# Kernel optimization log

Hardware: AMD Instinct MI355X
Metric: run time of the kernel (lower is better)

Reference implementation:

```python
import jax, jax.numpy as jnp
import numpy as np
import math

N_HEADS = 8
D_E = 64


def setup_inputs() -> dict:
    key = jax.random.key(0)
    k1, k2, k3 = jax.random.split(key, 3)
    B, C, L = 4, 512, 2048
    x = jax.random.normal(k1, (B, C, L), dtype=jnp.float32)
    # 1x1-conv (channel-mixing) projection shared by Q and K (the original
    # uses query_conv for both Q and K).
    W_q = jax.random.normal(k2, (N_HEADS * D_E, C), dtype=jnp.float32) * 0.02
    b_q = jax.random.normal(k3, (N_HEADS * D_E,), dtype=jnp.float32) * 0.02
    return {"x": x, "W_q": W_q, "b_q": b_q}


def reference(x, W_q, b_q):
    B, C, L = x.shape
    H, d_e = N_HEADS, D_E
    # 1x1 conv over channels: (B, H*d_e, L)
    qk = jnp.einsum('oc,bcl->bol', W_q, x) + b_q[None, :, None]
    # (B, H, L, d_e); K == Q per the original (both use query_conv)
    Q = qk.reshape(B, H, d_e, L).transpose(0, 1, 3, 2)
    K = Q
    scores = jnp.einsum('bhqd,bhkd->bhqk', Q, K) / math.sqrt(d_e)
    # causal mask: positions k > q masked to -inf (triu(diagonal=1) masked)
    causal = jnp.arange(L)[None, :] <= jnp.arange(L)[:, None]  # (L, L)
    scores = jnp.where(causal[None, None], scores, -jnp.inf)
    A = jax.nn.softmax(scores, axis=-1)  # (B, H, L, L)
    # values are the raw input sequence, (B, L, C)
    V = x.transpose(0, 2, 1)
    H_att = jnp.einsum('bhqk,bkc->bhqc', A, V)  # (B, H, L, C)
    out = H_att + V[:, None]                      # residual add per head
    # -> (B, H*C, L)
    return out.transpose(0, 1, 3, 2).reshape(B, H * C, L)
```

## Files before the change

kernel.cpp:

```cpp
#include <hip/hip_runtime.h>
#include <hip/hip_bf16.h>

#define B_ 4
#define C_ 512
#define L_ 2048
#define H_ 8
#define E_ 64
#define QSCALE 0.4246609f
#define NUNITS 1024

typedef __attribute__((ext_vector_type(8))) short bf16x8;
typedef __attribute__((ext_vector_type(4))) float f32x4;
typedef __attribute__((ext_vector_type(4))) unsigned short u16x4;

static __device__ __forceinline__ unsigned short f2bf(float f) {
    union { float f; unsigned u; } v; v.f = f;
    unsigned r = v.u + 0x7FFFu + ((v.u >> 16) & 1u);
    return (unsigned short)(r >> 16);
}

#define LBAR() do { asm volatile("s_waitcnt lgkmcnt(0)" ::: "memory"); \
                    __builtin_amdgcn_s_barrier(); } while (0)

__global__ __launch_bounds__(256) void prep_kernel(const float* __restrict__ x,
                                                   unsigned short* __restrict__ xb,
                                                   unsigned short* __restrict__ xt) {
    const int lt = blockIdx.x, ct = blockIdx.y, b = blockIdx.z;
    const int l0 = lt * 64, c0 = ct * 64;
    const int t = threadIdx.x;
    __shared__ unsigned short T[64 * 72];

    const int cl = t >> 2, lo = (t & 3) * 16;
    const float* src = x + ((size_t)(b * C_ + c0 + cl)) * L_ + l0 + lo;
    unsigned short u[16];
    #pragma unroll
    for (int j = 0; j < 16; j += 4) {
        float4 v = *reinterpret_cast<const float4*>(src + j);
        u[j] = f2bf(v.x); u[j + 1] = f2bf(v.y); u[j + 2] = f2bf(v.z); u[j + 3] = f2bf(v.w);
    }
    unsigned short* xbp = xb + ((size_t)(b * C_ + c0 + cl)) * L_ + l0 + lo;
    reinterpret_cast<uint4*>(xbp)[0] = reinterpret_cast<uint4*>(u)[0];
    reinterpret_cast<uint4*>(xbp)[1] = reinterpret_cast<uint4*>(u)[1];
    reinterpret_cast<uint4*>(&T[cl * 72 + lo])[0] = reinterpret_cast<uint4*>(u)[0];
    reinterpret_cast<uint4*>(&T[cl * 72 + lo + 8])[0] = reinterpret_cast<uint4*>(u)[1];
    __syncthreads();
    const int ll = t >> 2, co = (t & 3) * 16;
    unsigned short v16[16];
    #pragma unroll
    for (int j = 0; j < 16; ++j) v16[j] = T[(co + j) * 72 + ll];
    unsigned short* xtp = xt + ((size_t)b * L_ + l0 + ll) * C_ + c0 + co;
    reinterpret_cast<uint4*>(xtp)[0] = reinterpret_cast<uint4*>(v16)[0];
    reinterpret_cast<uint4*>(xtp)[1] = reinterpret_cast<uint4*>(v16)[1];
}

__global__ __launch_bounds__(256) void wcast_kernel(const float* __restrict__ W,
                                                    unsigned short* __restrict__ Wb) {
    const int i = blockIdx.x * 256 + threadIdx.x;
    float4 v = reinterpret_cast<const float4*>(W)[i];
    union { unsigned short u[4]; unsigned long long ll; } o;
    o.u[0] = f2bf(v.x); o.u[1] = f2bf(v.y); o.u[2] = f2bf(v.z); o.u[3] = f2bf(v.w);
    reinterpret_cast<unsigned long long*>(Wb)[i] = o.ll;
}

__global__ __launch_bounds__(256) void proj_kernel(const unsigned short* __restrict__ Wb,
                                                   const float* __restrict__ bq,
                                                   const unsigned short* __restrict__ xt,
                                                   unsigned short* __restrict__ qb) {
    const int lt = blockIdx.x, h = blockIdx.y, b = blockIdx.z;
    const int tid = threadIdx.x, w = tid >> 6, lane = tid & 63;
    const int lr = lane & 15, lg = lane >> 4;
    const int l = lt * 64 + w * 16 + lr;
    const int o0 = h * 64;

    f32x4 acc[4] = {};
    const unsigned short* xrow = xt + ((size_t)b * L_ + l) * C_;
    for (int ks = 0; ks < 16; ++ks) {
        bf16x8 bf = *reinterpret_cast<const bf16x8*>(xrow + ks * 32 + lg * 8);
        #pragma unroll
        for (int mt = 0; mt < 4; ++mt) {
            bf16x8 af = *reinterpret_cast<const bf16x8*>(Wb + (size_t)(o0 + mt * 16 + lr) * C_ + ks * 32 + lg * 8);
            acc[mt] = __builtin_amdgcn_mfma_f32_16x16x32_bf16(af, bf, acc[mt], 0, 0, 0);
        }
    }
    const int bh = b * H_ + h;
    unsigned short* qrow = qb + ((size_t)bh * L_ + l) * 64;
    #pragma unroll
    for (int mt = 0; mt < 4; ++mt) {
        const int e0 = mt * 16 + lg * 4;
        const float4 bb = *reinterpret_cast<const float4*>(bq + o0 + e0);
        union { unsigned short u[4]; unsigned long long ll; } o;
        o.u[0] = f2bf((acc[mt][0] + bb.x) * QSCALE);
        o.u[1] = f2bf((acc[mt][1] + bb.y) * QSCALE);
        o.u[2] = f2bf((acc[mt][2] + bb.z) * QSCALE);
        o.u[3] = f2bf((acc[mt][3] + bb.w) * QSCALE);
        *reinterpret_cast<unsigned long long*>(qrow + e0) = o.ll;
    }
}

#define LDV(KS)                                                                       \
    {                                                                                 \
        _Pragma("unroll")                                                             \
        for (int ct = 0; ct < 4; ++ct)                                                \
            pvv[ct] = *reinterpret_cast<const bf16x8*>(                               \
                Vbase + (size_t)(c0w + ct * 16 + lr) * L_ + k0 + (KS) * 32 + lg * 8); \
    }

#define PV_USE(KS)                                                                    \
    {                                                                                 \
        bf16x8 pa[4];                                                                 \
        _Pragma("unroll")                                                             \
        for (int mt = 0; mt < 4; ++mt) {                                              \
            const int row = mt * 16 + lr;                                             \
            const int g2 = ((KS) * 4 + lg) ^ lr;                                      \
            pa[mt] = *reinterpret_cast<const bf16x8*>(&Pb[row * 128 + (g2 << 3)]);    \
        }                                                                             \
        __builtin_amdgcn_s_setprio(1);                                                \
        _Pragma("unroll")                                                             \
        for (int mt = 0; mt < 4; ++mt)                                                \
            _Pragma("unroll")                                                         \
            for (int ct = 0; ct < 4; ++ct)                                            \
                acc[mt][ct] = __builtin_amdgcn_mfma_f32_16x16x32_bf16(                \
                    pa[mt], pvv[ct], acc[mt][ct], 0, 0, 0);                           \
        __builtin_amdgcn_s_setprio(0);                                                \
    }

__global__ __launch_bounds__(512, 4) void pv_kernel(const unsigned short* __restrict__ qb,
                                                    const unsigned short* __restrict__ xb,
                                                    float* __restrict__ out,
                                                    int* __restrict__ counter) {
    const int tid = threadIdx.x, w = tid >> 6, lane = tid & 63;
    const int lr = lane & 15, lg = lane >> 4;
    const int c0w = w * 64;

    __shared__ unsigned short Qt[64 * 64];
    __shared__ unsigned short P2[2][64 * 128];
    __shared__ float rsT[64][8];
    __shared__ int s_u;

    for (;;) {
        __syncthreads();
        if (tid == 0) s_u = atomicAdd(counter, 1);
        __syncthreads();
        const int u = s_u;
        if (u >= NUNITS) return;

        const int qt = 31 - (u >> 5);
        const int rr = u & 31;
        const int b = rr >> 3, h = rr & 7;
        const int q0 = qt * 64, qlim = q0 + 63;
        const int nkt = (q0 >> 7) + 1;
        const int bh = b * H_ + h;
        const unsigned short* Qbase = qb + (size_t)bh * L_ * 64;
        const unsigned short* Vbase = xb + (size_t)b * C_ * L_;

        {
            const int r = tid >> 3, g = tid & 7;
            bf16x8 v = *reinterpret_cast<const bf16x8*>(Qbase + (size_t)(q0 + r) * 64 + g * 8);
            *reinterpret_cast<bf16x8*>(&Qt[r * 64 + ((g ^ (r & 7)) << 3)]) = v;
        }

        bf16x8 pvv[4];
        f32x4 acc[4][4] = {};
        float rs[4] = {0.f, 0.f, 0.f, 0.f};

        LBAR();

        #pragma unroll 1
        for (int kt = 0; kt < nkt; ++kt) {
            const int k0 = kt * 128;
            const int ksmax = min(4, ((qlim - k0) >> 5) + 1);
            unsigned short* Pb = (unsigned short*)P2[kt & 1];
            const bool active = (k0 + (w & ~1) * 16) <= qlim;

            LDV(0)

            if (active) {
                const size_t krow = (size_t)(k0 + w * 16 + lr) * 64;
                bf16x8 kb0 = *reinterpret_cast<const bf16x8*>(Qbase + krow + lg * 8);
                bf16x8 kb1 = *reinterpret_cast<const bf16x8*>(Qbase + krow + 32 + lg * 8);
                f32x4 z[4];
                #pragma unroll
                for (int nt = 0; nt < 4; ++nt) {
                    bf16x8 aq0 = *reinterpret_cast<const bf16x8*>(&Qt[(nt * 16 + lr) * 64 + ((lg ^ (lr & 7)) << 3)]);
                    bf16x8 aq1 = *reinterpret_cast<const bf16x8*>(&Qt[(nt * 16 + lr) * 64 + (((4 + lg) ^ (lr & 7)) << 3)]);
                    f32x4 zz = {};
                    zz = __builtin_amdgcn_mfma_f32_16x16x32_bf16(kb0, aq0, zz, 0, 0, 0);
                    zz = __builtin_amdgcn_mfma_f32_16x16x32_bf16(kb1, aq1, zz, 0, 0, 0);
                    z[nt] = zz;
                }
                const int kbase = k0 + w * 16 + lg * 4;
                #pragma unroll
                for (int nt = 0; nt < 4; ++nt) {
                    const int q = q0 + nt * 16 + lr;
                    const float p0 = (kbase + 0 <= q) ? exp2f(z[nt][0]) : 0.f;
                    const float p1 = (kbase + 1 <= q) ? exp2f(z[nt][1]) : 0.f;
                    const float p2 = (kbase + 2 <= q) ? exp2f(z[nt][2]) : 0.f;
                    const float p3 = (kbase + 3 <= q) ? exp2f(z[nt][3]) : 0.f;
                    rs[nt] += (p0 + p1) + (p2 + p3);
                    unsigned r01, r23;
                    asm("v_cvt_pk_bf16_f32 %0, %1, %2" : "=v"(r01) : "v"(p0), "v"(p1));
                    asm("v_cvt_pk_bf16_f32 %0, %1, %2" : "=v"(r23) : "v"(p2), "v"(p3));
                    const int row = nt * 16 + lr;
                    const int col = w * 16 + lg * 4;
                    const int gg = (col >> 3) ^ lr;
                    const unsigned long long pk = ((unsigned long long)r23 << 32) | r01;
                    *reinterpret_cast<unsigned long long*>(&Pb[row * 128 + (gg << 3) + (col & 7)]) = pk;
                }
            }
            LBAR();

            PV_USE(0)
            LDV(1)
            PV_USE(1)
            if (ksmax == 4) {
                LDV(2)
                PV_USE(2)
                LDV(3)
                PV_USE(3)
            }
        }

        #pragma unroll
        for (int nt = 0; nt < 4; ++nt) {
            float t0 = __shfl_xor(rs[nt], 16); rs[nt] += t0;
            float t1 = __shfl_xor(rs[nt], 32); rs[nt] += t1;
        }
        if (lg == 0) {
            #pragma unroll
            for (int nt = 0; nt < 4; ++nt) rsT[nt * 16 + lr][w] = rs[nt];
        }
        LBAR();
        float li[16];
        #pragma unroll
        for (int mt = 0; mt < 4; ++mt)
            #pragma unroll
            for (int r = 0; r < 4; ++r) {
                const int row = mt * 16 + lg * 4 + r;
                const f32x4 s0 = *reinterpret_cast<const f32x4*>(&rsT[row][0]);
                const f32x4 s1 = *reinterpret_cast<const f32x4*>(&rsT[row][4]);
                li[mt * 4 + r] = 1.f / (((s0[0] + s0[1]) + (s0[2] + s0[3])) + ((s1[0] + s1[1]) + (s1[2] + s1[3])));
            }

        const unsigned short* xres = xb + (size_t)b * C_ * L_;
        float* ob = out + (size_t)bh * C_ * L_;
        #pragma unroll
        for (int ct = 0; ct < 4; ++ct) {
            const int c = c0w + ct * 16 + lr;
            #pragma unroll
            for (int mt = 0; mt < 4; ++mt) {
                const int lbase = q0 + mt * 16 + lg * 4;
                const u16x4 rv = __builtin_nontemporal_load(
                    reinterpret_cast<const u16x4*>(xres + (size_t)c * L_ + lbase));
                f32x4 o;
                o[0] = acc[mt][ct][0] * li[mt * 4 + 0] + __uint_as_float((unsigned)rv[0] << 16);
                o[1] = acc[mt][ct][1] * li[mt * 4 + 1] + __uint_as_float((unsigned)rv[1] << 16);
                o[2] = acc[mt][ct][2] * li[mt * 4 + 2] + __uint_as_float((unsigned)rv[2] << 16);
                o[3] = acc[mt][ct][3] * li[mt * 4 + 3] + __uint_as_float((unsigned)rv[3] << 16);
                __builtin_nontemporal_store(o, reinterpret_cast<f32x4*>(ob + (size_t)c * L_ + lbase));
            }
        }
    }
}

extern "C" void kernel_launch(void* const* d_in, const int* in_sizes, int n_in,
                              void* d_out, int out_size, void* d_ws, size_t ws_size,
                              hipStream_t stream) {
    const float* x  = (const float*)d_in[0];
    const float* Wq = (const float*)d_in[1];
    const float* bq = (const float*)d_in[2];
    float* out = (float*)d_out;

    unsigned short* xb   = (unsigned short*)d_ws;
    unsigned short* xt   = xb + (size_t)B_ * C_ * L_;
    unsigned short* qbuf = xt + (size_t)B_ * L_ * C_;
    unsigned short* Wb   = qbuf + (size_t)B_ * H_ * L_ * E_;
    int* counter = (int*)(Wb + (size_t)H_ * E_ * C_);

    (void)hipMemsetAsync(counter, 0, 4, stream);
    prep_kernel<<<dim3(32, 8, 4), 256, 0, stream>>>(x, xb, xt);
    wcast_kernel<<<dim3(256), 256, 0, stream>>>(Wq, Wb);
    proj_kernel<<<dim3(32, 8, 4), 256, 0, stream>>>(Wb, bq, xt, qbuf);
    pv_kernel<<<dim3(768), 512, 0, stream>>>(qbuf, xb, out, counter);
}
```

Baseline: 290.5 us.

## Double attention query tile to 128 rows using 1024-thread blocks

The fused score/PV kernel now handles 128 query rows per work unit with 16 waves instead of 64 rows with 8 waves. Each wave covers 32 channels over all 128 rows, so every V tile loaded from global memory is reused across twice as many queries. The causal-diagonal partial-tile logic is dropped, so diagonal tiles are computed in full with masking. The larger shared-memory footprint and 1024-thread blocks lower the number of resident blocks per CU, and the grid shrinks to 256 persistent blocks.

```diff
diff --git a/kernel.cpp b/kernel.cpp
--- a/kernel.cpp
+++ b/kernel.cpp
@@ -7,7 +7,7 @@
 #define H_ 8
 #define E_ 64
 #define QSCALE 0.4246609f
-#define NUNITS 1024
+#define NUNITS 512
 
 typedef __attribute__((ext_vector_type(8))) short bf16x8;
 typedef __attribute__((ext_vector_type(4))) float f32x4;
@@ -97,44 +97,49 @@
     }
 }
 
-#define LDV(KS)                                                                       \
-    {                                                                                 \
-        _Pragma("unroll")                                                             \
-        for (int ct = 0; ct < 4; ++ct)                                                \
-            pvv[ct] = *reinterpret_cast<const bf16x8*>(                               \
-                Vbase + (size_t)(c0w + ct * 16 + lr) * L_ + k0 + (KS) * 32 + lg * 8); \
-    }
-
-#define PV_USE(KS)                                                                    \
-    {                                                                                 \
-        bf16x8 pa[4];                                                                 \
-        _Pragma("unroll")                                                             \
-        for (int mt = 0; mt < 4; ++mt) {                                              \
-            const int row = mt * 16 + lr;                                             \
-            const int g2 = ((KS) * 4 + lg) ^ lr;                                      \
-            pa[mt] = *reinterpret_cast<const bf16x8*>(&Pb[row * 128 + (g2 << 3)]);    \
-        }                                                                             \
-        __builtin_amdgcn_s_setprio(1);                                                \
-        _Pragma("unroll")                                                             \
-        for (int mt = 0; mt < 4; ++mt)                                                \
-            _Pragma("unroll")                                                         \
-            for (int ct = 0; ct < 4; ++ct)                                            \
-                acc[mt][ct] = __builtin_amdgcn_mfma_f32_16x16x32_bf16(                \
-                    pa[mt], pvv[ct], acc[mt][ct], 0, 0, 0);                           \
-        __builtin_amdgcn_s_setprio(0);                                                \
-    }
-
-__global__ __launch_bounds__(512, 4) void pv_kernel(const unsigned short* __restrict__ qb,
-                                                    const unsigned short* __restrict__ xb,
-                                                    float* __restrict__ out,
-                                                    int* __restrict__ counter) {
+#define LDV(KS)                                                                        \
+    {                                                                                  \
+        _Pragma("unroll")                                                              \
+        for (int ct = 0; ct < 2; ++ct)                                                 \
+            pvv[ct] = *reinterpret_cast<const bf16x8*>(                                \
+                Vbase + (size_t)(c0w + ct * 16 + lr) * L_ + k0 + (KS) * 32 + lg * 8);  \
+    }
+
+#define PV_USE(KS)                                                                     \
+    {                                                                                  \
+        _Pragma("unroll")                                                              \
+        for (int half = 0; half < 2; ++half) {                                         \
+            bf16x8 pa[4];                                                              \
+            _Pragma("unroll")                                                          \
+            for (int mt = 0; mt < 4; ++mt) {                                           \
+                const int row = half * 64 + mt * 16 + lr;                              \
+                const int g2 = ((KS) * 4 + lg) ^ lr;                                   \
+                pa[mt] = *reinterpret_cast<const bf16x8*>(&Pb[row * 128 + (g2 << 3)]); \
+            }                                                                          \
+            __builtin_amdgcn_s_setprio(1);                                             \
+            _Pragma("unroll")                                                          \
+            for (int mt = 0; mt < 4; ++mt)                                             \
+                _Pragma("unroll")                                                      \
+                for (int ct = 0; ct < 2; ++ct)                                         \
+                    acc[half * 4 + mt][ct] = __builtin_amdgcn_mfma_f32_16x16x32_bf16(  \
+                        pa[mt], pvv[ct], acc[half * 4 + mt][ct], 0, 0, 0);             \
+            __builtin_amdgcn_s_setprio(0);                                             \
+        }                                                                              \
+    }
+
+__global__ __launch_bounds__(1024, 4) void pv_kernel(const unsigned short* __restrict__ qb,
+                                                     const unsigned short* __restrict__ xb,
+                                                     float* __restrict__ out,
+                                                     int* __restrict__ counter) {
     const int tid = threadIdx.x, w = tid >> 6, lane = tid & 63;
     const int lr = lane & 15, lg = lane >> 4;
-    const int c0w = w * 64;
-
-    __shared__ unsigned short Qt[64 * 64];
-    __shared__ unsigned short P2[2][64 * 128];
-    __shared__ float rsT[64][8];
+    const int sq = w >> 3;
+    const int wk = w & 7;
+    const int c0w = w * 32;
+
+    __shared__ unsigned short Qt[128 * 64];
+    __shared__ unsigned short P2[2][128 * 128];
+    __shared__ float rsT[128][8];
     __shared__ int s_u;
 
     for (;;) {
@@ -144,11 +149,11 @@
         const int u = s_u;
         if (u >= NUNITS) return;
 
-        const int qt = 31 - (u >> 5);
+        const int qt = 15 - (u >> 5);
         const int rr = u & 31;
         const int b = rr >> 3, h = rr & 7;
-        const int q0 = qt * 64, qlim = q0 + 63;
-        const int nkt = (q0 >> 7) + 1;
+        const int q0 = qt * 128;
+        const int nkt = qt + 1;
         const int bh = b * H_ + h;
         const unsigned short* Qbase = qb + (size_t)bh * L_ * 64;
         const unsigned short* Vbase = xb + (size_t)b * C_ * L_;
@@ -159,8 +164,8 @@
             *reinterpret_cast<bf16x8*>(&Qt[r * 64 + ((g ^ (r & 7)) << 3)]) = v;
         }
 
-        bf16x8 pvv[4];
-        f32x4 acc[4][4] = {};
+        bf16x8 pvv[2];
+        f32x4 acc[8][2] = {};
         float rs[4] = {0.f, 0.f, 0.f, 0.f};
 
         LBAR();
@@ -168,56 +173,45 @@
         #pragma unroll 1
         for (int kt = 0; kt < nkt; ++kt) {
             const int k0 = kt * 128;
-            const int ksmax = min(4, ((qlim - k0) >> 5) + 1);
             unsigned short* Pb = (unsigned short*)P2[kt & 1];
-            const bool active = (k0 + (w & ~1) * 16) <= qlim;
-
+
+            const size_t krow = (size_t)(k0 + wk * 16 + lr) * 64;
+            bf16x8 kb0 = *reinterpret_cast<const bf16x8*>(Qbase + krow + lg * 8);
+            bf16x8 kb1 = *reinterpret_cast<const bf16x8*>(Qbase + krow + 32 + lg * 8);
             LDV(0)
 
-            if (active) {
-                const size_t krow = (size_t)(k0 + w * 16 + lr) * 64;
-                bf16x8 kb0 = *reinterpret_cast<const bf16x8*>(Qbase + krow + lg * 8);
-                bf16x8 kb1 = *reinterpret_cast<const bf16x8*>(Qbase + krow + 32 + lg * 8);
-                f32x4 z[4];
-                #pragma unroll
-                for (int nt = 0; nt < 4; ++nt) {
-                    bf16x8 aq0 = *reinterpret_cast<const bf16x8*>(&Qt[(nt * 16 + lr) * 64 + ((lg ^ (lr & 7)) << 3)]);
-                    bf16x8 aq1 = *reinterpret_cast<const bf16x8*>(&Qt[(nt * 16 + lr) * 64 + (((4 + lg) ^ (lr & 7)) << 3)]);
-                    f32x4 zz = {};
-                    zz = __builtin_amdgcn_mfma_f32_16x16x32_bf16(kb0, aq0, zz, 0, 0, 0);
-                    zz = __builtin_amdgcn_mfma_f32_16x16x32_bf16(kb1, aq1, zz, 0, 0, 0);
-                    z[nt] = zz;
-                }
-                const int kbase = k0 + w * 16 + lg * 4;
-                #pragma unroll
-                for (int nt = 0; nt < 4; ++nt) {
-                    const int q = q0 + nt * 16 + lr;
-                    const float p0 = (kbase + 0 <= q) ? exp2f(z[nt][0]) : 0.f;
-                    const float p1 = (kbase + 1 <= q) ? exp2f(z[nt][1]) : 0.f;
-                    const float p2 = (kbase + 2 <= q) ? exp2f(z[nt][2]) : 0.f;
-                    const float p3 = (kbase + 3 <= q) ? exp2f(z[nt][3]) : 0.f;
-                    rs[nt] += (p0 + p1) + (p2 + p3);
-                    unsigned r01, r23;
-                    asm("v_cvt_pk_bf16_f32 %0, %1, %2" : "=v"(r01) : "v"(p0), "v"(p1));
-                    asm("v_cvt_pk_bf16_f32 %0, %1, %2" : "=v"(r23) : "v"(p2), "v"(p3));
-                    const int row = nt * 16 + lr;
-                    const int col = w * 16 + lg * 4;
-                    const int gg = (col >> 3) ^ lr;
-                    const unsigned long long pk = ((unsigned long long)r23 << 32) | r01;
-                    *reinterpret_cast<unsigned long long*>(&Pb[row * 128 + (gg << 3) + (col & 7)]) = pk;
-                }
+            const int kbase = k0 + wk * 16 + lg * 4;
+            #pragma unroll
+            for (int nt = 0; nt < 4; ++nt) {
+                const int qrow = sq * 64 + nt * 16 + lr;
+                bf16x8 aq0 = *reinterpret_cast<const bf16x8*>(&Qt[qrow * 64 + ((lg ^ (lr & 7)) << 3)]);
+                bf16x8 aq1 = *reinterpret_cast<const bf16x8*>(&Qt[qrow * 64 + (((4 + lg) ^ (lr & 7)) << 3)]);
+                f32x4 z = {};
+                z = __builtin_amdgcn_mfma_f32_16x16x32_bf16(kb0, aq0, z, 0, 0, 0);
+                z = __builtin_amdgcn_mfma_f32_16x16x32_bf16(kb1, aq1, z, 0, 0, 0);
+                const int q = q0 + qrow;
+                const float p0 = (kbase + 0 <= q) ? exp2f(z[0]) : 0.f;
+                const float p1 = (kbase + 1 <= q) ? exp2f(z[1]) : 0.f;
+                const float p2 = (kbase + 2 <= q) ? exp2f(z[2]) : 0.f;
+                const float p3 = (kbase + 3 <= q) ? exp2f(z[3]) : 0.f;
+                rs[nt] += (p0 + p1) + (p2 + p3);
+                unsigned r01, r23;
+                asm("v_cvt_pk_bf16_f32 %0, %1, %2" : "=v"(r01) : "v"(p0), "v"(p1));
+                asm("v_cvt_pk_bf16_f32 %0, %1, %2" : "=v"(r23) : "v"(p2), "v"(p3));
+                const int col = wk * 16 + lg * 4;
+                const int gg = (col >> 3) ^ lr;
+                const unsigned long long pk = ((unsigned long long)r23 << 32) | r01;
+                *reinterpret_cast<unsigned long long*>(&Pb[qrow * 128 + (gg << 3) + (col & 7)]) = pk;
             }
             LBAR();
 
             PV_USE(0)
             LDV(1)
             PV_USE(1)
-            if (ksmax == 4) {
-                LDV(2)
-                PV_USE(2)
-                LDV(3)
-                PV_USE(3)
-            }
+            LDV(2)
+            PV_USE(2)
+            LDV(3)
+            PV_USE(3)
         }
 
         #pragma unroll
@@ -227,35 +221,33 @@
         }
         if (lg == 0) {
             #pragma unroll
-            for (int nt = 0; nt < 4; ++nt) rsT[nt * 16 + lr][w] = rs[nt];
+            for (int nt = 0; nt < 4; ++nt) rsT[sq * 64 + nt * 16 + lr][wk] = rs[nt];
         }
         LBAR();
-        float li[16];
-        #pragma unroll
-        for (int mt = 0; mt < 4; ++mt)
-            #pragma unroll
-            for (int r = 0; r < 4; ++r) {
-                const int row = mt * 16 + lg * 4 + r;
-                const f32x4 s0 = *reinterpret_cast<const f32x4*>(&rsT[row][0]);
-                const f32x4 s1 = *reinterpret_cast<const f32x4*>(&rsT[row][4]);
-                li[mt * 4 + r] = 1.f / (((s0[0] + s0[1]) + (s0[2] + s0[3])) + ((s1[0] + s1[1]) + (s1[2] + s1[3])));
-            }
 
         const unsigned short* xres = xb + (size_t)b * C_ * L_;
         float* ob = out + (size_t)bh * C_ * L_;
         #pragma unroll
-        for (int ct = 0; ct < 4; ++ct) {
-            const int c = c0w + ct * 16 + lr;
-            #pragma unroll
-            for (int mt = 0; mt < 4; ++mt) {
-                const int lbase = q0 + mt * 16 + lg * 4;
+        for (int mt = 0; mt < 8; ++mt) {
+            const int rowb = mt * 16 + lg * 4;
+            f32x4 li;
+            #pragma unroll
+            for (int r = 0; r < 4; ++r) {
+                const f32x4 s0 = *reinterpret_cast<const f32x4*>(&rsT[rowb + r][0]);
+                const f32x4 s1 = *reinterpret_cast<const f32x4*>(&rsT[rowb + r][4]);
+                li[r] = 1.f / (((s0[0] + s0[1]) + (s0[2] + s0[3])) + ((s1[0] + s1[1]) + (s1[2] + s1[3])));
+            }
+            const int lbase = q0 + rowb;
+            #pragma unroll
+            for (int ct = 0; ct < 2; ++ct) {
+                const int c = c0w + ct * 16 + lr;
                 const u16x4 rv = __builtin_nontemporal_load(
                     reinterpret_cast<const u16x4*>(xres + (size_t)c * L_ + lbase));
                 f32x4 o;
-                o[0] = acc[mt][ct][0] * li[mt * 4 + 0] + __uint_as_float((unsigned)rv[0] << 16);
-                o[1] = acc[mt][ct][1] * li[mt * 4 + 1] + __uint_as_float((unsigned)rv[1] << 16);
-                o[2] = acc[mt][ct][2] * li[mt * 4 + 2] + __uint_as_float((unsigned)rv[2] << 16);
-                o[3] = acc[mt][ct][3] * li[mt * 4 + 3] + __uint_as_float((unsigned)rv[3] << 16);
+                o[0] = acc[mt][ct][0] * li[0] + __uint_as_float((unsigned)rv[0] << 16);
+                o[1] = acc[mt][ct][1] * li[1] + __uint_as_float((unsigned)rv[1] << 16);
+                o[2] = acc[mt][ct][2] * li[2] + __uint_as_float((unsigned)rv[2] << 16);
+                o[3] = acc[mt][ct][3] * li[3] + __uint_as_float((unsigned)rv[3] << 16);
                 __builtin_nontemporal_store(o, reinterpret_cast<f32x4*>(ob + (size_t)c * L_ + lbase));
             }
         }
@@ -280,5 +272,5 @@
     prep_kernel<<<dim3(32, 8, 4), 256, 0, stream>>>(x, xb, xt);
     wcast_kernel<<<dim3(256), 256, 0, stream>>>(Wq, Wb);
     proj_kernel<<<dim3(32, 8, 4), 256, 0, stream>>>(Wb, bq, xt, qbuf);
-    pv_kernel<<<dim3(768), 512, 0, stream>>>(qbuf, xb, out, counter);
-}
+    pv_kernel<<<dim3(256), 1024, 0, stream>>>(qbuf, xb, out, counter);
+}
```

New measurement: 287.5 us. Within noise of the previous version (-1.0%).

## Split attention work units across channel halves with 4-wave blocks

Applied to the files above, without the earlier changes.

The fused attention kernel now assigns each work unit to one (batch, head, query tile, channel half), doubling the unit count and using 256-thread blocks with four waves. Each wave computes 32 key columns of the score tile instead of 16, and the double-buffered P tile is replaced by a single buffer with an extra barrier after the PV step. This aims to improve load balance and occupancy under the persistent atomic scheduler. In exchange the QK^T scores and exponentials are recomputed twice per query tile, once per channel half.

```diff
diff --git a/kernel.cpp b/kernel.cpp
--- a/kernel.cpp
+++ b/kernel.cpp
@@ -7,7 +7,7 @@
 #define H_ 8
 #define E_ 64
 #define QSCALE 0.4246609f
-#define NUNITS 1024
+#define NUNITS 2048
 
 typedef __attribute__((ext_vector_type(8))) short bf16x8;
 typedef __attribute__((ext_vector_type(4))) float f32x4;
@@ -97,44 +97,40 @@
     }
 }
 
-#define LDV(KS)                                                                       \
-    {                                                                                 \
-        _Pragma("unroll")                                                             \
-        for (int ct = 0; ct < 4; ++ct)                                                \
-            pvv[ct] = *reinterpret_cast<const bf16x8*>(                               \
-                Vbase + (size_t)(c0w + ct * 16 + lr) * L_ + k0 + (KS) * 32 + lg * 8); \
-    }
-
-#define PV_USE(KS)                                                                    \
-    {                                                                                 \
-        bf16x8 pa[4];                                                                 \
-        _Pragma("unroll")                                                             \
-        for (int mt = 0; mt < 4; ++mt) {                                              \
-            const int row = mt * 16 + lr;                                             \
-            const int g2 = ((KS) * 4 + lg) ^ lr;                                      \
-            pa[mt] = *reinterpret_cast<const bf16x8*>(&Pb[row * 128 + (g2 << 3)]);    \
-        }                                                                             \
-        __builtin_amdgcn_s_setprio(1);                                                \
-        _Pragma("unroll")                                                             \
-        for (int mt = 0; mt < 4; ++mt)                                                \
-            _Pragma("unroll")                                                         \
-            for (int ct = 0; ct < 4; ++ct)                                            \
-                acc[mt][ct] = __builtin_amdgcn_mfma_f32_16x16x32_bf16(                \
-                    pa[mt], pvv[ct], acc[mt][ct], 0, 0, 0);                           \
-        __builtin_amdgcn_s_setprio(0);                                                \
-    }
-
-__global__ __launch_bounds__(512, 4) void pv_kernel(const unsigned short* __restrict__ qb,
+#define PV_STEP(S)                                                                        \
+    {                                                                                     \
+        bf16x8 vf[4];                                                                     \
+        _Pragma("unroll")                                                                 \
+        for (int ct = 0; ct < 4; ++ct)                                                    \
+            vf[ct] = *reinterpret_cast<const bf16x8*>(                                    \
+                Vbase + (size_t)(c0w + ct * 16 + lr) * L_ + k0 + (S) * 32 + lg * 8);      \
+        bf16x8 pa[4];                                                                     \
+        _Pragma("unroll")                                                                 \
+        for (int qs = 0; qs < 4; ++qs) {                                                  \
+            const int row = qs * 16 + lr;                                                 \
+            const int g2 = ((S) * 4 + lg) ^ (lr & 7);                                     \
+            pa[qs] = *reinterpret_cast<const bf16x8*>(&P[row * 128 + (g2 << 3)]);         \
+        }                                                                                 \
+        __builtin_amdgcn_s_setprio(1);                                                    \
+        _Pragma("unroll")                                                                 \
+        for (int qs = 0; qs < 4; ++qs)                                                    \
+            _Pragma("unroll")                                                             \
+            for (int ct = 0; ct < 4; ++ct)                                                \
+                acc[qs][ct] = __builtin_amdgcn_mfma_f32_16x16x32_bf16(                    \
+                    pa[qs], vf[ct], acc[qs][ct], 0, 0, 0);                                \
+        __builtin_amdgcn_s_setprio(0);                                                    \
+    }
+
+__global__ __launch_bounds__(256, 4) void pv_kernel(const unsigned short* __restrict__ qb,
                                                     const unsigned short* __restrict__ xb,
                                                     float* __restrict__ out,
                                                     int* __restrict__ counter) {
     const int tid = threadIdx.x, w = tid >> 6, lane = tid & 63;
     const int lr = lane & 15, lg = lane >> 4;
-    const int c0w = w * 64;
 
     __shared__ unsigned short Qt[64 * 64];
-    __shared__ unsigned short P2[2][64 * 128];
-    __shared__ float rsT[64][8];
+    __shared__ unsigned short P[64 * 128];
+    __shared__ float rsT[64][4];
     __shared__ int s_u;
 
     for (;;) {
@@ -144,22 +140,26 @@
         const int u = s_u;
         if (u >= NUNITS) return;
 
-        const int qt = 31 - (u >> 5);
-        const int rr = u & 31;
-        const int b = rr >> 3, h = rr & 7;
+        const int qt = 31 - (u >> 6);
+        const int rr = u & 63;
+        const int bh = rr >> 1, ch = rr & 1;
+        const int b = bh >> 3;
         const int q0 = qt * 64, qlim = q0 + 63;
         const int nkt = (q0 >> 7) + 1;
-        const int bh = b * H_ + h;
+        const int c0w = ch * 256 + w * 64;
         const unsigned short* Qbase = qb + (size_t)bh * L_ * 64;
         const unsigned short* Vbase = xb + (size_t)b * C_ * L_;
 
         {
-            const int r = tid >> 3, g = tid & 7;
-            bf16x8 v = *reinterpret_cast<const bf16x8*>(Qbase + (size_t)(q0 + r) * 64 + g * 8);
-            *reinterpret_cast<bf16x8*>(&Qt[r * 64 + ((g ^ (r & 7)) << 3)]) = v;
-        }
-
-        bf16x8 pvv[4];
+            const int r = tid >> 2, seg = tid & 3;
+            const unsigned short* src = Qbase + (size_t)(q0 + r) * 64 + seg * 16;
+            bf16x8 v0 = *reinterpret_cast<const bf16x8*>(src);
+            bf16x8 v1 = *reinterpret_cast<const bf16x8*>(src + 8);
+            const int g0 = seg * 2, g1 = seg * 2 + 1;
+            *reinterpret_cast<bf16x8*>(&Qt[r * 64 + ((g0 ^ (r & 7)) << 3)]) = v0;
+            *reinterpret_cast<bf16x8*>(&Qt[r * 64 + ((g1 ^ (r & 7)) << 3)]) = v1;
+        }
+
         f32x4 acc[4][4] = {};
         float rs[4] = {0.f, 0.f, 0.f, 0.f};
 
@@ -169,93 +169,87 @@
         for (int kt = 0; kt < nkt; ++kt) {
             const int k0 = kt * 128;
             const int ksmax = min(4, ((qlim - k0) >> 5) + 1);
-            unsigned short* Pb = (unsigned short*)P2[kt & 1];
-            const bool active = (k0 + (w & ~1) * 16) <= qlim;
-
-            LDV(0)
+            const bool active = (w < ksmax);
+            const int kw0 = k0 + w * 32;
 
             if (active) {
-                const size_t krow = (size_t)(k0 + w * 16 + lr) * 64;
-                bf16x8 kb0 = *reinterpret_cast<const bf16x8*>(Qbase + krow + lg * 8);
-                bf16x8 kb1 = *reinterpret_cast<const bf16x8*>(Qbase + krow + 32 + lg * 8);
-                f32x4 z[4];
+                bf16x8 kb[2][2];
                 #pragma unroll
-                for (int nt = 0; nt < 4; ++nt) {
-                    bf16x8 aq0 = *reinterpret_cast<const bf16x8*>(&Qt[(nt * 16 + lr) * 64 + ((lg ^ (lr & 7)) << 3)]);
-                    bf16x8 aq1 = *reinterpret_cast<const bf16x8*>(&Qt[(nt * 16 + lr) * 64 + (((4 + lg) ^ (lr & 7)) << 3)]);
-                    f32x4 zz = {};
-                    zz = __builtin_amdgcn_mfma_f32_16x16x32_bf16(kb0, aq0, zz, 0, 0, 0);
-                    zz = __builtin_amdgcn_mfma_f32_16x16x32_bf16(kb1, aq1, zz, 0, 0, 0);
-                    z[nt] = zz;
+                for (int ksub = 0; ksub < 2; ++ksub) {
+                    const size_t krow = (size_t)(kw0 + ksub * 16 + lr) * 64;
+                    kb[ksub][0] = *reinterpret_cast<const bf16x8*>(Qbase + krow + lg * 8);
+                    kb[ksub][1] = *reinterpret_cast<const bf16x8*>(Qbase + krow + 32 + lg * 8);
                 }
-                const int kbase = k0 + w * 16 + lg * 4;
                 #pragma unroll
-                for (int nt = 0; nt < 4; ++nt) {
-                    const int q = q0 + nt * 16 + lr;
-                    const float p0 = (kbase + 0 <= q) ? exp2f(z[nt][0]) : 0.f;
-                    const float p1 = (kbase + 1 <= q) ? exp2f(z[nt][1]) : 0.f;
-                    const float p2 = (kbase + 2 <= q) ? exp2f(z[nt][2]) : 0.f;
-                    const float p3 = (kbase + 3 <= q) ? exp2f(z[nt][3]) : 0.f;
-                    rs[nt] += (p0 + p1) + (p2 + p3);
-                    unsigned r01, r23;
-                    asm("v_cvt_pk_bf16_f32 %0, %1, %2" : "=v"(r01) : "v"(p0), "v"(p1));
-                    asm("v_cvt_pk_bf16_f32 %0, %1, %2" : "=v"(r23) : "v"(p2), "v"(p3));
-                    const int row = nt * 16 + lr;
-                    const int col = w * 16 + lg * 4;
-                    const int gg = (col >> 3) ^ lr;
-                    const unsigned long long pk = ((unsigned long long)r23 << 32) | r01;
-                    *reinterpret_cast<unsigned long long*>(&Pb[row * 128 + (gg << 3) + (col & 7)]) = pk;
+                for (int qs = 0; qs < 4; ++qs) {
+                    const int qrow = qs * 16 + lr;
+                    bf16x8 qf0 = *reinterpret_cast<const bf16x8*>(&Qt[qrow * 64 + ((lg ^ (qrow & 7)) << 3)]);
+                    bf16x8 qf1 = *reinterpret_cast<const bf16x8*>(&Qt[qrow * 64 + (((4 + lg) ^ (qrow & 7)) << 3)]);
+                    const int q = q0 + qrow;
+                    #pragma unroll
+                    for (int ksub = 0; ksub < 2; ++ksub) {
+                        f32x4 z = {};
+                        z = __builtin_amdgcn_mfma_f32_16x16x32_bf16(kb[ksub][0], qf0, z, 0, 0, 0);
+                        z = __builtin_amdgcn_mfma_f32_16x16x32_bf16(kb[ksub][1], qf1, z, 0, 0, 0);
+                        const int kbase = kw0 + ksub * 16 + lg * 4;
+                        const float p0 = (kbase + 0 <= q) ? exp2f(z[0]) : 0.f;
+                        const float p1 = (kbase + 1 <= q) ? exp2f(z[1]) : 0.f;
+                        const float p2 = (kbase + 2 <= q) ? exp2f(z[2]) : 0.f;
+                        const float p3 = (kbase + 3 <= q) ? exp2f(z[3]) : 0.f;
+                        rs[qs] += (p0 + p1) + (p2 + p3);
+                        unsigned r01, r23;
+                        asm("v_cvt_pk_bf16_f32 %0, %1, %2" : "=v"(r01) : "v"(p0), "v"(p1));
+                        asm("v_cvt_pk_bf16_f32 %0, %1, %2" : "=v"(r23) : "v"(p2), "v"(p3));
+                        const int kl = w * 32 + ksub * 16 + lg * 4;
+                        const int g = (kl >> 3) ^ (qrow & 7);
+                        const unsigned long long pk = ((unsigned long long)r23 << 32) | r01;
+                        *reinterpret_cast<unsigned long long*>(&P[qrow * 128 + (g << 3) + (kl & 7)]) = pk;
+                    }
                 }
             }
             LBAR();
 
-            PV_USE(0)
-            LDV(1)
-            PV_USE(1)
+            PV_STEP(0)
+            PV_STEP(1)
             if (ksmax == 4) {
-                LDV(2)
-                PV_USE(2)
-                LDV(3)
-                PV_USE(3)
-            }
+                PV_STEP(2)
+                PV_STEP(3)
+            }
+            LBAR();
         }
 
         #pragma unroll
-        for (int nt = 0; nt < 4; ++nt) {
-            float t0 = __shfl_xor(rs[nt], 16); rs[nt] += t0;
-            float t1 = __shfl_xor(rs[nt], 32); rs[nt] += t1;
+        for (int qs = 0; qs < 4; ++qs) {
+            float t0 = __shfl_xor(rs[qs], 16); rs[qs] += t0;
+            float t1 = __shfl_xor(rs[qs], 32); rs[qs] += t1;
         }
         if (lg == 0) {
             #pragma unroll
-            for (int nt = 0; nt < 4; ++nt) rsT[nt * 16 + lr][w] = rs[nt];
+            for (int qs = 0; qs < 4; ++qs) rsT[qs * 16 + lr][w] = rs[qs];
         }
         LBAR();
-        float li[16];
-        #pragma unroll
-        for (int mt = 0; mt < 4; ++mt)
-            #pragma unroll
-            for (int r = 0; r < 4; ++r) {
-                const int row = mt * 16 + lg * 4 + r;
-                const f32x4 s0 = *reinterpret_cast<const f32x4*>(&rsT[row][0]);
-                const f32x4 s1 = *reinterpret_cast<const f32x4*>(&rsT[row][4]);
-                li[mt * 4 + r] = 1.f / (((s0[0] + s0[1]) + (s0[2] + s0[3])) + ((s1[0] + s1[1]) + (s1[2] + s1[3])));
-            }
 
         const unsigned short* xres = xb + (size_t)b * C_ * L_;
         float* ob = out + (size_t)bh * C_ * L_;
         #pragma unroll
-        for (int ct = 0; ct < 4; ++ct) {
-            const int c = c0w + ct * 16 + lr;
+        for (int qs = 0; qs < 4; ++qs) {
+            f32x4 li;
             #pragma unroll
-            for (int mt = 0; mt < 4; ++mt) {
-                const int lbase = q0 + mt * 16 + lg * 4;
+            for (int r = 0; r < 4; ++r) {
+                const f32x4 s4 = *reinterpret_cast<const f32x4*>(&rsT[qs * 16 + lg * 4 + r][0]);
+                li[r] = 1.f / ((s4[0] + s4[1]) + (s4[2] + s4[3]));
+            }
+            const int lbase = q0 + qs * 16 + lg * 4;
+            #pragma unroll
+            for (int ct = 0; ct < 4; ++ct) {
+                const int c = c0w + ct * 16 + lr;
                 const u16x4 rv = __builtin_nontemporal_load(
                     reinterpret_cast<const u16x4*>(xres + (size_t)c * L_ + lbase));
                 f32x4 o;
-                o[0] = acc[mt][ct][0] * li[mt * 4 + 0] + __uint_as_float((unsigned)rv[0] << 16);
-                o[1] = acc[mt][ct][1] * li[mt * 4 + 1] + __uint_as_float((unsigned)rv[1] << 16);
-                o[2] = acc[mt][ct][2] * li[mt * 4 + 2] + __uint_as_float((unsigned)rv[2] << 16);
-                o[3] = acc[mt][ct][3] * li[mt * 4 + 3] + __uint_as_float((unsigned)rv[3] << 16);
+                o[0] = acc[qs][ct][0] * li[0] + __uint_as_float((unsigned)rv[0] << 16);
+                o[1] = acc[qs][ct][1] * li[1] + __uint_as_float((unsigned)rv[1] << 16);
+                o[2] = acc[qs][ct][2] * li[2] + __uint_as_float((unsigned)rv[2] << 16);
+                o[3] = acc[qs][ct][3] * li[3] + __uint_as_float((unsigned)rv[3] << 16);
                 __builtin_nontemporal_store(o, reinterpret_cast<f32x4*>(ob + (size_t)c * L_ + lbase));
             }
         }
@@ -280,5 +274,5 @@
     prep_kernel<<<dim3(32, 8, 4), 256, 0, stream>>>(x, xb, xt);
     wcast_kernel<<<dim3(256), 256, 0, stream>>>(Wq, Wb);
     proj_kernel<<<dim3(32, 8, 4), 256, 0, stream>>>(Wb, bq, xt, qbuf);
-    pv_kernel<<<dim3(768), 512, 0, stream>>>(qbuf, xb, out, counter);
-}
+    pv_kernel<<<dim3(1024), 256, 0, stream>>>(qbuf, xb, out, counter);
+}
```

Measured after the change: 379.8 us. 1.31x slower.

## Warp-specialize pv_kernel into score-producer and PV-consumer waves with double buffering

Applied to the files above, without the earlier changes.

Splits each 768-thread block into 4 producer waves, which compute QK^T scores, exp and row sums into a double-buffered P tile one k-tile ahead, and 8 consumer waves, which run the PV MFMAs and the epilogue. Consumer V loads are also double-buffered in registers so the next slice is prefetched during the current MFMAs. The aim is to overlap the softmax/score stage with the PV matmul rather than serializing them each iteration. In exchange, the grid drops to 256 persistent blocks with launch bounds 768,3, which changes occupancy and register limits, and block-wide barriers still couple the two roles.

```diff
diff --git a/kernel.cpp b/kernel.cpp
--- a/kernel.cpp
+++ b/kernel.cpp
@@ -97,44 +97,91 @@
     }
 }
 
-#define LDV(KS)                                                                       \
-    {                                                                                 \
-        _Pragma("unroll")                                                             \
-        for (int ct = 0; ct < 4; ++ct)                                                \
-            pvv[ct] = *reinterpret_cast<const bf16x8*>(                               \
-                Vbase + (size_t)(c0w + ct * 16 + lr) * L_ + k0 + (KS) * 32 + lg * 8); \
-    }
-
-#define PV_USE(KS)                                                                    \
-    {                                                                                 \
-        bf16x8 pa[4];                                                                 \
-        _Pragma("unroll")                                                             \
-        for (int mt = 0; mt < 4; ++mt) {                                              \
-            const int row = mt * 16 + lr;                                             \
-            const int g2 = ((KS) * 4 + lg) ^ lr;                                      \
-            pa[mt] = *reinterpret_cast<const bf16x8*>(&Pb[row * 128 + (g2 << 3)]);    \
-        }                                                                             \
-        __builtin_amdgcn_s_setprio(1);                                                \
-        _Pragma("unroll")                                                             \
-        for (int mt = 0; mt < 4; ++mt)                                                \
-            _Pragma("unroll")                                                         \
-            for (int ct = 0; ct < 4; ++ct)                                            \
-                acc[mt][ct] = __builtin_amdgcn_mfma_f32_16x16x32_bf16(                \
-                    pa[mt], pvv[ct], acc[mt][ct], 0, 0, 0);                           \
-        __builtin_amdgcn_s_setprio(0);                                                \
-    }
-
-__global__ __launch_bounds__(512, 4) void pv_kernel(const unsigned short* __restrict__ qb,
+#define PRODUCE(BUF, PK0)                                                                        \
+    {                                                                                            \
+        const int kw0 = (PK0) + sw * 32;                                                         \
+        if (kw0 <= qlim) {                                                                       \
+            bf16x8 kb00, kb01, kb10, kb11;                                                       \
+            {                                                                                    \
+                const size_t kr0 = (size_t)(kw0 + lr) * 64;                                      \
+                const size_t kr1 = (size_t)(kw0 + 16 + lr) * 64;                                 \
+                kb00 = *reinterpret_cast<const bf16x8*>(Qbase + kr0 + lg * 8);                   \
+                kb01 = *reinterpret_cast<const bf16x8*>(Qbase + kr0 + 32 + lg * 8);              \
+                kb10 = *reinterpret_cast<const bf16x8*>(Qbase + kr1 + lg * 8);                   \
+                kb11 = *reinterpret_cast<const bf16x8*>(Qbase + kr1 + 32 + lg * 8);              \
+            }                                                                                    \
+            unsigned short* Pw = (unsigned short*)P2[BUF];                                       \
+            _Pragma("unroll")                                                                    \
+            for (int nt = 0; nt < 4; ++nt) {                                                     \
+                const int qrow = nt * 16 + lr;                                                   \
+                bf16x8 aq0 = *reinterpret_cast<const bf16x8*>(&Qt[qrow * 64 + ((lg ^ (lr & 7)) << 3)]);       \
+                bf16x8 aq1 = *reinterpret_cast<const bf16x8*>(&Qt[qrow * 64 + (((4 + lg) ^ (lr & 7)) << 3)]); \
+                const int q = q0 + qrow;                                                         \
+                _Pragma("unroll")                                                                \
+                for (int ksub = 0; ksub < 2; ++ksub) {                                           \
+                    f32x4 z = {};                                                                \
+                    z = __builtin_amdgcn_mfma_f32_16x16x32_bf16(ksub ? kb10 : kb00, aq0, z, 0, 0, 0); \
+                    z = __builtin_amdgcn_mfma_f32_16x16x32_bf16(ksub ? kb11 : kb01, aq1, z, 0, 0, 0); \
+                    const int kbase = kw0 + ksub * 16 + lg * 4;                                  \
+                    const float p0 = (kbase + 0 <= q) ? exp2f(z[0]) : 0.f;                       \
+                    const float p1 = (kbase + 1 <= q) ? exp2f(z[1]) : 0.f;                       \
+                    const float p2 = (kbase + 2 <= q) ? exp2f(z[2]) : 0.f;                       \
+                    const float p3 = (kbase + 3 <= q) ? exp2f(z[3]) : 0.f;                       \
+                    rs[nt] += (p0 + p1) + (p2 + p3);                                             \
+                    unsigned r01, r23;                                                           \
+                    asm("v_cvt_pk_bf16_f32 %0, %1, %2" : "=v"(r01) : "v"(p0), "v"(p1));          \
+                    asm("v_cvt_pk_bf16_f32 %0, %1, %2" : "=v"(r23) : "v"(p2), "v"(p3));          \
+                    const int kl = sw * 32 + ksub * 16 + lg * 4;                                 \
+                    const int gg = (kl >> 3) ^ lr;                                               \
+                    const unsigned long long pk = ((unsigned long long)r23 << 32) | r01;         \
+                    *reinterpret_cast<unsigned long long*>(&Pw[qrow * 128 + (gg << 3) + (kl & 7)]) = pk; \
+                }                                                                                \
+            }                                                                                    \
+        }                                                                                        \
+    }
+
+#define LDVB(BANK, KOFF)                                                                \
+    {                                                                                   \
+        _Pragma("unroll")                                                               \
+        for (int ct = 0; ct < 4; ++ct)                                                  \
+            pvv[BANK][ct] = *reinterpret_cast<const bf16x8*>(                           \
+                Vbase + (size_t)(c0w + ct * 16 + lr) * L_ + (KOFF) + lg * 8);           \
+    }
+
+#define PV_STEP(CUR, NXT, S)                                                            \
+    {                                                                                   \
+        const int nl = ((S) + 1 < ksmax) ? k0 + ((S) + 1) * 32 : k0 + 128;              \
+        LDVB(NXT, nl)                                                                   \
+        bf16x8 pa[4];                                                                   \
+        _Pragma("unroll")                                                               \
+        for (int mt = 0; mt < 4; ++mt) {                                                \
+            const int row = mt * 16 + lr;                                               \
+            const int g2 = ((S) * 4 + lg) ^ lr;                                         \
+            pa[mt] = *reinterpret_cast<const bf16x8*>(&Pb[row * 128 + (g2 << 3)]);      \
+        }                                                                               \
+        __builtin_amdgcn_s_setprio(1);                                                  \
+        _Pragma("unroll")                                                               \
+        for (int mt = 0; mt < 4; ++mt)                                                  \
+            _Pragma("unroll")                                                           \
+            for (int ct = 0; ct < 4; ++ct)                                              \
+                acc[mt][ct] = __builtin_amdgcn_mfma_f32_16x16x32_bf16(                  \
+                    pa[mt], pvv[CUR][ct], acc[mt][ct], 0, 0, 0);                        \
+        __builtin_amdgcn_s_setprio(0);                                                  \
+    }
+
+__global__ __launch_bounds__(768, 3) void pv_kernel(const unsigned short* __restrict__ qb,
                                                     const unsigned short* __restrict__ xb,
                                                     float* __restrict__ out,
                                                     int* __restrict__ counter) {
     const int tid = threadIdx.x, w = tid >> 6, lane = tid & 63;
     const int lr = lane & 15, lg = lane >> 4;
-    const int c0w = w * 64;
+    const bool isS = (w < 4);
+    const int sw = w;
+    const int c0w = (w - 4) * 64;
 
     __shared__ unsigned short Qt[64 * 64];
     __shared__ unsigned short P2[2][64 * 128];
-    __shared__ float rsT[64][8];
+    __shared__ float rsT[64][4];
     __shared__ int s_u;
 
     for (;;) {
@@ -153,110 +200,80 @@
         const unsigned short* Qbase = qb + (size_t)bh * L_ * 64;
         const unsigned short* Vbase = xb + (size_t)b * C_ * L_;
 
-        {
+        if (tid < 512) {
             const int r = tid >> 3, g = tid & 7;
             bf16x8 v = *reinterpret_cast<const bf16x8*>(Qbase + (size_t)(q0 + r) * 64 + g * 8);
             *reinterpret_cast<bf16x8*>(&Qt[r * 64 + ((g ^ (r & 7)) << 3)]) = v;
         }
 
-        bf16x8 pvv[4];
         f32x4 acc[4][4] = {};
         float rs[4] = {0.f, 0.f, 0.f, 0.f};
-
+        bf16x8 pvv[2][4];
+
+        LBAR();
+
+        if (isS) {
+            PRODUCE(0, 0)
+        } else {
+            LDVB(0, 0)
+        }
         LBAR();
 
         #pragma unroll 1
         for (int kt = 0; kt < nkt; ++kt) {
             const int k0 = kt * 128;
-            const int ksmax = min(4, ((qlim - k0) >> 5) + 1);
-            unsigned short* Pb = (unsigned short*)P2[kt & 1];
-            const bool active = (k0 + (w & ~1) * 16) <= qlim;
-
-            LDV(0)
-
-            if (active) {
-                const size_t krow = (size_t)(k0 + w * 16 + lr) * 64;
-                bf16x8 kb0 = *reinterpret_cast<const bf16x8*>(Qbase + krow + lg * 8);
-                bf16x8 kb1 = *reinterpret_cast<const bf16x8*>(Qbase + krow + 32 + lg * 8);
-                f32x4 z[4];
-                #pragma unroll
-                for (int nt = 0; nt < 4; ++nt) {
-                    bf16x8 aq0 = *reinterpret_cast<const bf16x8*>(&Qt[(nt * 16 + lr) * 64 + ((lg ^ (lr & 7)) << 3)]);
-                    bf16x8 aq1 = *reinterpret_cast<const bf16x8*>(&Qt[(nt * 16 + lr) * 64 + (((4 + lg) ^ (lr & 7)) << 3)]);
-                    f32x4 zz = {};
-                    zz = __builtin_amdgcn_mfma_f32_16x16x32_bf16(kb0, aq0, zz, 0, 0, 0);
-                    zz = __builtin_amdgcn_mfma_f32_16x16x32_bf16(kb1, aq1, zz, 0, 0, 0);
-                    z[nt] = zz;
-                }
-                const int kbase = k0 + w * 16 + lg * 4;
-                #pragma unroll
-                for (int nt = 0; nt < 4; ++nt) {
-                    const int q = q0 + nt * 16 + lr;
-                    const float p0 = (kbase + 0 <= q) ? exp2f(z[nt][0]) : 0.f;
-                    const float p1 = (kbase + 1 <= q) ? exp2f(z[nt][1]) : 0.f;
-                    const float p2 = (kbase + 2 <= q) ? exp2f(z[nt][2]) : 0.f;
-                    const float p3 = (kbase + 3 <= q) ? exp2f(z[nt][3]) : 0.f;
-                    rs[nt] += (p0 + p1) + (p2 + p3);
-                    unsigned r01, r23;
-                    asm("v_cvt_pk_bf16_f32 %0, %1, %2" : "=v"(r01) : "v"(p0), "v"(p1));
-                    asm("v_cvt_pk_bf16_f32 %0, %1, %2" : "=v"(r23) : "v"(p2), "v"(p3));
-                    const int row = nt * 16 + lr;
-                    const int col = w * 16 + lg * 4;
-                    const int gg = (col >> 3) ^ lr;
-                    const unsigned long long pk = ((unsigned long long)r23 << 32) | r01;
-                    *reinterpret_cast<unsigned long long*>(&Pb[row * 128 + (gg << 3) + (col & 7)]) = pk;
+            if (isS) {
+                if (kt + 1 < nkt) PRODUCE((kt + 1) & 1, k0 + 128)
+            } else {
+                const unsigned short* Pb = (const unsigned short*)P2[kt & 1];
+                const int ksmax = min(4, ((qlim - k0) >> 5) + 1);
+                PV_STEP(0, 1, 0)
+                PV_STEP(1, 0, 1)
+                if (ksmax == 4) {
+                    PV_STEP(0, 1, 2)
+                    PV_STEP(1, 0, 3)
                 }
             }
             LBAR();
-
-            PV_USE(0)
-            LDV(1)
-            PV_USE(1)
-            if (ksmax == 4) {
-                LDV(2)
-                PV_USE(2)
-                LDV(3)
-                PV_USE(3)
+        }
+
+        if (isS) {
+            #pragma unroll
+            for (int nt = 0; nt < 4; ++nt) {
+                float t0 = __shfl_xor(rs[nt], 16); rs[nt] += t0;
+                float t1 = __shfl_xor(rs[nt], 32); rs[nt] += t1;
             }
-        }
-
-        #pragma unroll
-        for (int nt = 0; nt < 4; ++nt) {
-            float t0 = __shfl_xor(rs[nt], 16); rs[nt] += t0;
-            float t1 = __shfl_xor(rs[nt], 32); rs[nt] += t1;
-        }
-        if (lg == 0) {
-            #pragma unroll
-            for (int nt = 0; nt < 4; ++nt) rsT[nt * 16 + lr][w] = rs[nt];
+            if (lg == 0) {
+                #pragma unroll
+                for (int nt = 0; nt < 4; ++nt) rsT[nt * 16 + lr][sw] = rs[nt];
+            }
         }
         LBAR();
-        float li[16];
-        #pragma unroll
-        for (int mt = 0; mt < 4; ++mt)
-            #pragma unroll
-            for (int r = 0; r < 4; ++r) {
-                const int row = mt * 16 + lg * 4 + r;
-                const f32x4 s0 = *reinterpret_cast<const f32x4*>(&rsT[row][0]);
-                const f32x4 s1 = *reinterpret_cast<const f32x4*>(&rsT[row][4]);
-                li[mt * 4 + r] = 1.f / (((s0[0] + s0[1]) + (s0[2] + s0[3])) + ((s1[0] + s1[1]) + (s1[2] + s1[3])));
-            }
-
-        const unsigned short* xres = xb + (size_t)b * C_ * L_;
-        float* ob = out + (size_t)bh * C_ * L_;
-        #pragma unroll
-        for (int ct = 0; ct < 4; ++ct) {
-            const int c = c0w + ct * 16 + lr;
+
+        if (!isS) {
+            const unsigned short* xres = xb + (size_t)b * C_ * L_;
+            float* ob = out + (size_t)bh * C_ * L_;
             #pragma unroll
             for (int mt = 0; mt < 4; ++mt) {
+                f32x4 li;
+                #pragma unroll
+                for (int r = 0; r < 4; ++r) {
+                    const f32x4 s4 = *reinterpret_cast<const f32x4*>(&rsT[mt * 16 + lg * 4 + r][0]);
+                    li[r] = 1.f / ((s4[0] + s4[1]) + (s4[2] + s4[3]));
+                }
                 const int lbase = q0 + mt * 16 + lg * 4;
-                const u16x4 rv = __builtin_nontemporal_load(
-                    reinterpret_cast<const u16x4*>(xres + (size_t)c * L_ + lbase));
-                f32x4 o;
-                o[0] = acc[mt][ct][0] * li[mt * 4 + 0] + __uint_as_float((unsigned)rv[0] << 16);
-                o[1] = acc[mt][ct][1] * li[mt * 4 + 1] + __uint_as_float((unsigned)rv[1] << 16);
-                o[2] = acc[mt][ct][2] * li[mt * 4 + 2] + __uint_as_float((unsigned)rv[2] << 16);
-                o[3] = acc[mt][ct][3] * li[mt * 4 + 3] + __uint_as_float((unsigned)rv[3] << 16);
-                __builtin_nontemporal_store(o, reinterpret_cast<f32x4*>(ob + (size_t)c * L_ + lbase));
+                #pragma unroll
+                for (int ct = 0; ct < 4; ++ct) {
+                    const int c = c0w + ct * 16 + lr;
+                    const u16x4 rv = __builtin_nontemporal_load(
+                        reinterpret_cast<const u16x4*>(xres + (size_t)c * L_ + lbase));
+                    f32x4 o;
+                    o[0] = acc[mt][ct][0] * li[0] + __uint_as_float((unsigned)rv[0] << 16);
+                    o[1] = acc[mt][ct][1] * li[1] + __uint_as_float((unsigned)rv[1] << 16);
+                    o[2] = acc[mt][ct][2] * li[2] + __uint_as_float((unsigned)rv[2] << 16);
+                    o[3] = acc[mt][ct][3] * li[3] + __uint_as_float((unsigned)rv[3] << 16);
+                    __builtin_nontemporal_store(o, reinterpret_cast<f32x4*>(ob + (size_t)c * L_ + lbase));
+                }
             }
         }
     }
@@ -280,5 +297,5 @@
     prep_kernel<<<dim3(32, 8, 4), 256, 0, stream>>>(x, xb, xt);
     wcast_kernel<<<dim3(256), 256, 0, stream>>>(Wq, Wb);
     proj_kernel<<<dim3(32, 8, 4), 256, 0, stream>>>(Wb, bq, xt, qbuf);
-    pv_kernel<<<dim3(768), 512, 0, stream>>>(qbuf, xb, out, counter);
-}
+    pv_kernel<<<dim3(256), 768, 0, stream>>>(qbuf, xb, out, counter);
+}
```

After: 344.5 us. +18.6%, slower.
